# Kernel tuning notes

Measured on AMD Instinct MI355X. Metric: run time of the kernel, lower is better.

## Reference

```python
import jax, jax.numpy as jnp
from jax import lax
import numpy as np

B, C, H, W = 8, 192, 56, 56
N = H * W
K_CLUSTERS = 16   # num_centroids
K_NBRS = 9        # kNN neighbors
FACTOR = 2
COUT = C * FACTOR # hidden channels of graph conv
CPE_K = 7         # depthwise CPE kernel (odd)


def setup_inputs() -> dict:
    key = jax.random.key(0)
    ks = jax.random.split(key, 12)
    s = 0.02
    return {
        "x": jax.random.normal(ks[0], (B, C, H, W), jnp.float32),
        "labels": jax.random.randint(ks[1], (B, N), 0, K_CLUSTERS, jnp.int32),
        "cpe_w": jax.random.normal(ks[2], (C, 1, CPE_K, CPE_K), jnp.float32) * s,
        "cpe_b": jnp.zeros((C,), jnp.float32),
        "fc1_w": jax.random.normal(ks[3], (C, C), jnp.float32) * s,
        "fc1_b": jnp.zeros((C,), jnp.float32),
        "nn_v_w": jax.random.normal(ks[4], (2 * C, COUT), jnp.float32) * s,
        "nn_v_b": jnp.zeros((COUT,), jnp.float32),
        "nn_c_w": jax.random.normal(ks[5], (2 * C, COUT), jnp.float32) * s,
        "nn_c_b": jnp.zeros((COUT,), jnp.float32),
        "fc2_w": jax.random.normal(ks[6], (COUT, C), jnp.float32) * s,
        "fc2_b": jnp.zeros((C,), jnp.float32),
    }


def reference(x, labels, cpe_w, cpe_b, fc1_w, fc1_b, nn_v_w, nn_v_b,
              nn_c_w, nn_c_b, fc2_w, fc2_b):
    Bx, Cx, Hx, Wx = x.shape
    n = Hx * Wx
    shortcut = x
    # --- Conditional Position Encoding: depthwise conv + residual ---
    pe = lax.conv_general_dilated(
        x, cpe_w, (1, 1), "SAME", feature_group_count=Cx,
        dimension_numbers=("NCHW", "OIHW", "NCHW"))
    x = pe + cpe_b[None, :, None, None] + x
    # --- fc1: 1x1 conv ---
    xf = jnp.einsum("bchw,cd->bdhw", x, fc1_w) + fc1_b[None, :, None, None]
    xn = xf.reshape(Bx, Cx, n).transpose(0, 2, 1)  # [B,N,C]
    # --- organize_and_map: stable sort nodes by cluster label ---
    order = jnp.argsort(labels, axis=1)            # sorted pos -> orig idx (stable)
    mapping = jnp.argsort(order, axis=1)           # orig idx -> sorted pos
    xs = jnp.take_along_axis(xn, order[:, :, None], axis=1)  # [B,N,C]
    ls = jnp.take_along_axis(labels, order, axis=1)          # [B,N]
    # --- kNN on l2-normalized feats, restricted to same cluster ---
    xe = xs / jnp.maximum(jnp.linalg.norm(xs, axis=-1, keepdims=True), 1e-12)
    sq = jnp.sum(xe * xe, axis=-1)                 # [B,N]
    d2 = sq[:, :, None] + sq[:, None, :] - 2.0 * jnp.einsum("bnc,bmc->bnm", xe, xe)
    same = ls[:, :, None] == ls[:, None, :]        # [B,N,N] cluster mask
    d2 = jnp.where(same, d2, jnp.inf)
    _, nbr = lax.top_k(-d2, K_NBRS)                # [B,N,k] nearest in-cluster
    valid = jnp.take_along_axis(same, nbr, axis=2) # False when cluster < k
    # --- vertex edge conv: max_j MLP([x_i, x_j - x_i]) ---
    xj = jax.vmap(lambda xb, nb: xb[nb])(xs, nbr)  # [B,N,k,C]
    xi = xs[:, :, None, :]
    msg = jnp.concatenate([jnp.broadcast_to(xi, xj.shape), xj - xi], axis=-1)
    h = jax.nn.gelu(msg @ nn_v_w + nn_v_b)         # [B,N,k,COUT]
    h = jnp.where(valid[..., None], h, -jnp.inf)   # self is always valid
    hv = jnp.max(h, axis=2)                        # [B,N,COUT]
    # --- centroid edge conv over cluster centers (fully connected per image) ---
    onehot = (ls[:, :, None] == jnp.arange(K_CLUSTERS)[None, None, :]).astype(xs.dtype)
    cnt = jnp.maximum(onehot.sum(axis=1), 1.0)     # [B,K]
    cen = jnp.einsum("bnk,bnc->bkc", onehot, xs) / cnt[:, :, None]
    ci = cen[:, :, None, :]
    cj = cen[:, None, :, :]
    cmsg = jnp.concatenate(
        [jnp.broadcast_to(ci, (Bx, K_CLUSTERS, K_CLUSTERS, Cx)), cj - ci], axis=-1)
    hc = jnp.max(jax.nn.gelu(cmsg @ nn_c_w + nn_c_b), axis=2)  # [B,K,COUT]
    hcn = jax.vmap(lambda hb, lb: hb[lb])(hc, ls)  # scatter center feat to nodes
    hn = hv + hcn                                  # [B,N,COUT]
    # --- unshuffle back to original raster order ---
    out_nodes = jnp.take_along_axis(hn, mapping[:, :, None], axis=1)
    # --- fc2: 1x1 conv back to C, residual ---
    y = out_nodes @ fc2_w + fc2_b                  # [B,N,C]
    y = y.transpose(0, 2, 1).reshape(Bx, Cx, Hx, Wx)
    return y + shortcut
```

## Files before the change

### kernel.cpp

```cpp
#include <hip/hip_runtime.h>
#include <math.h>

#define NB 8
#define NC 192
#define NH 56
#define NW 56
#define NN 3136
#define NK 16
#define KNB 9
#define NCOUT 384
#define LPMAX 320
#define DSTRIDE 320
#define DSLOT (320 * 320)

#define FLT_INF __builtin_inff()

typedef short s16x8 __attribute__((ext_vector_type(8)));
typedef _Float16 f16x8 __attribute__((ext_vector_type(8)));
typedef float f32x4 __attribute__((ext_vector_type(4)));
typedef unsigned short us8 __attribute__((ext_vector_type(8)));
typedef unsigned short us4 __attribute__((ext_vector_type(4)));

__device__ __forceinline__ float gelu_t(float x) {
    const float k0 = 0.7978845608028654f;
    float u = k0 * (x + 0.044715f * x * x * x);
    float sg = __builtin_amdgcn_rcpf(1.0f + __expf(-2.0f * u));
    return x * sg;
}

__device__ __forceinline__ unsigned short f2bf(float f) {
    unsigned u = __float_as_uint(f);
    u += 0x7fff + ((u >> 16) & 1);
    return (unsigned short)(u >> 16);
}

__device__ __forceinline__ float bf2f(unsigned short h) {
    return __uint_as_float(((unsigned)h) << 16);
}


#define FRONT_CONV_BLOCKS (NB * NC)
#define FRONT_ORDER_BLOCKS (NB * NK)
#define FRONT_WCVT_BLOCKS 288
__global__ __launch_bounds__(256) void front_kernel(
    const float* __restrict__ X, const float* __restrict__ W7, const float* __restrict__ bias,
    unsigned short* __restrict__ xpe,
    const int* __restrict__ labels, int* __restrict__ order, int* __restrict__ mapping,
    int* __restrict__ lsv, int* __restrict__ cntk, int* __restrict__ offk,
    const float* __restrict__ Wf1, const float* __restrict__ Wv, const float* __restrict__ Wf2,
    unsigned short* __restrict__ wf1, unsigned short* __restrict__ wfpmq,
    unsigned short* __restrict__ wfq, unsigned short* __restrict__ wf2) {
    __shared__ float tile[62 * 62];
    __shared__ float wl[49];
    int bid = blockIdx.x;
    int tid = threadIdx.x;
    if (bid < FRONT_CONV_BLOCKS) {
        int bc = (bid & 7) * NC + (bid >> 3);
        int c = bc % NC;
        const float* Xp = X + (size_t)bc * NN;
        if (tid < 49) wl[tid] = W7[(size_t)c * 49 + tid];
        for (int idx = tid; idx < 62 * 62; idx += 256) {
            int ty = idx / 62, tx = idx % 62;
            int gy = ty - 3, gx = tx - 3;
            float v = 0.0f;
            if (gy >= 0 && gy < NH && gx >= 0 && gx < NW) v = Xp[gy * NW + gx];
            tile[idx] = v;
        }
        __syncthreads();
        float cb = bias[c];
        for (int g = tid; g < (NN / 4); g += 256) {
            int y = g / (NW / 4), x0 = (g % (NW / 4)) * 4;
            float a0 = 0.f, a1 = 0.f, a2 = 0.f, a3 = 0.f;
#pragma unroll
            for (int dy = 0; dy < 7; ++dy) {
                const float* tr = &tile[(y + dy) * 62 + x0];
#pragma unroll
                for (int dx = 0; dx < 7; ++dx) {
                    float wv = wl[dy * 7 + dx];
                    a0 += tr[dx] * wv;
                    a1 += tr[dx + 1] * wv;
                    a2 += tr[dx + 2] * wv;
                    a3 += tr[dx + 3] * wv;
                }
            }
            const float* rr = &tile[(y + 3) * 62 + x0 + 3];
            us4 o;
            o[0] = f2bf(a0 + cb + rr[0]);
            o[1] = f2bf(a1 + cb + rr[1]);
            o[2] = f2bf(a2 + cb + rr[2]);
            o[3] = f2bf(a3 + cb + rr[3]);
            *(us4*)(xpe + (size_t)bc * NN + y * NW + x0) = o;
        }
    } else if (bid < FRONT_CONV_BLOCKS + FRONT_ORDER_BLOCKS) {
        if (tid >= 64) return;
        int idx = bid - FRONT_CONV_BLOCKS;
        int b = idx >> 4;
        int k = idx & 15;
        int lane = tid;
        const int* lb = labels + (size_t)b * NN;
        int cntLess = 0, cntEq = 0;
        for (int n0 = 0; n0 < NN; n0 += 64) {
            int lab = lb[n0 + lane] & 15;
            cntLess += __popcll(__ballot(lab < k));
            cntEq += __popcll(__ballot(lab == k));
        }
        int base = cntLess;
        int run = 0;
        for (int n0 = 0; n0 < NN; n0 += 64) {
            int n = n0 + lane;
            int lab = lb[n] & 15;
            bool p = (lab == k);
            unsigned long long mask = __ballot(p);
            int rank = __popcll(mask & ((1ull << lane) - 1ull));
            if (p) {
                int pos = base + run + rank;
                order[b * NN + pos] = n;
                mapping[b * NN + n] = pos;
                lsv[b * NN + pos] = k;
            }
            run += __popcll(mask);
        }
        if (lane == 0) {
            offk[b * NK + k] = base;
            cntk[b * NK + k] = cntEq;
        }
    } else {
        int u = bid - (FRONT_CONV_BLOCKS + FRONT_ORDER_BLOCKS);
        int nt = u % 6, kc = (u / 6) % 12, z = u / 72;
        const float* W;
        unsigned short* Bf;
        int ldw, rowoff, KC, NT;
        bool diff = false;
        if (z == 0) { W = Wf1; Bf = wf1; ldw = NC; rowoff = 0; KC = 6; NT = 3; }
        else if (z == 1) { W = Wv; Bf = wfpmq; ldw = NCOUT; rowoff = 0; KC = 6; NT = 6; diff = true; }
        else if (z == 2) { W = Wv; Bf = wfq; ldw = NCOUT; rowoff = NC; KC = 6; NT = 6; }
        else { W = Wf2; Bf = wf2; ldw = NC; rowoff = 0; KC = 12; NT = 3; }
        if (nt >= NT || kc >= KC) return;
        int c = tid >> 6, l = tid & 63;
        int n = l & 15, q = l >> 4;
        int col = nt * 64 + c * 16 + n;
        int krow = rowoff + kc * 32 + q * 8;
        unsigned short pack[8];
#pragma unroll
        for (int j = 0; j < 8; ++j) {
            float v = W[(size_t)(krow + j) * ldw + col];
            if (diff) v -= W[(size_t)(NC + krow + j) * ldw + col];
            pack[j] = f2bf(v);
        }
        *(us8*)(Bf + ((((size_t)nt * KC + kc) * 4 + c) * 64 + l) * 8) = *(const us8*)pack;
    }
}

__global__ __launch_bounds__(256) void tcvt_kernel(const unsigned short* __restrict__ xpe,
                                                   unsigned short* __restrict__ Af) {
    __shared__ unsigned short t[32][72];
    int lin = ((int)blockIdx.z * 6 + blockIdx.y) * 49 + blockIdx.x;
    int b = lin & 7, pos = lin >> 3;
    int kc = pos / 49, nx = pos % 49;
    int n0 = nx * 64;
    int tid = threadIdx.x;
    int cl = tid >> 3, nl = (tid & 7) * 8;
    const unsigned short* src = xpe + ((size_t)b * NC + kc * 32 + cl) * NN + n0 + nl;
    *(us8*)&t[cl][nl] = *(const us8*)src;
    __syncthreads();
    int w = tid >> 6, l = tid & 63;
    int m = l & 15, q = l >> 4;
    int nloc = w * 16 + m;
    unsigned short pack[8];
#pragma unroll
    for (int j = 0; j < 8; ++j) pack[j] = t[q * 8 + j][nloc];
    int sg = nx * 4 + w;
    *(us8*)(Af + (size_t)b * NN * NC + (((size_t)sg * 6 + kc) * 64 + l) * 8) =
        *(const us8*)pack;
}

template <int KC>
__global__ __launch_bounds__(256) void gemm_mfma(const unsigned short* __restrict__ Af,
                                                 size_t aStride,
                                                 const unsigned short* __restrict__ Bf,
                                                 const float* __restrict__ bias,
                                                 float* __restrict__ C, size_t cStride,
                                                 int ldc, unsigned short* __restrict__ Cfrag,
                                                 const int* __restrict__ rowmap) {
    int NX = gridDim.x;
    int lin = ((int)blockIdx.z * 49 + blockIdx.y) * NX + blockIdx.x;
    int b = lin & 7, pos = lin >> 3;
    int bx = pos % NX, by = pos / NX;
    int w = threadIdx.x >> 6, lane = threadIdx.x & 63;
    int sg = by * 4 + w;
    int n0 = bx * 64;
    const unsigned short* Ap = Af + (size_t)b * aStride + ((size_t)sg * KC * 64 + lane) * 8;
    const unsigned short* Bp = Bf + ((size_t)bx * KC * 256 + lane) * 8;
    f32x4 acc[4] = {};
#pragma unroll
    for (int kc = 0; kc < KC; ++kc) {
        s16x8 a = *(const s16x8*)(Ap + kc * 512);
#pragma unroll
        for (int c = 0; c < 4; ++c) {
            s16x8 bv = *(const s16x8*)(Bp + kc * 2048 + c * 512);
            acc[c] = __builtin_amdgcn_mfma_f32_16x16x32_bf16(a, bv, acc[c], 0, 0, 0);
        }
    }
    int col0 = lane & 15, rq = lane >> 4;
    float* Cb = C + (size_t)b * cStride;
    int kcd = ldc >> 5;
#pragma unroll
    for (int r = 0; r < 4; ++r) {
        int grow = sg * 16 + rq * 4 + r;
        int orow = rowmap ? rowmap[(size_t)b * NN + grow] : grow;
#pragma unroll
        for (int c = 0; c < 4; ++c) {
            int col = n0 + c * 16 + col0;
            float v = acc[c][r];
            if (bias) v += bias[col];
            Cb[(size_t)orow * ldc + col] = v;
            if (Cfrag) {
                int s2 = orow >> 4, m2 = orow & 15;
                int kc2 = col >> 5, q2 = (col >> 3) & 3, j2 = col & 7;
                Cfrag[(size_t)b * cStride +
                      (((size_t)s2 * kcd + kc2) * 64 + q2 * 16 + m2) * 8 + j2] = f2bf(v);
            }
        }
    }
}

template <int KC>
__global__ __launch_bounds__(256) void gemm_mfma_pq(const unsigned short* __restrict__ Af,
                                                    size_t aStride,
                                                    const unsigned short* __restrict__ B1,
                                                    const unsigned short* __restrict__ B2,
                                                    const float* __restrict__ bias,
                                                    unsigned short* __restrict__ PmQ,
                                                    unsigned short* __restrict__ Qh,
                                                    size_t cStride, int ldc) {
    int lin = ((int)blockIdx.z * 49 + blockIdx.y) * 6 + blockIdx.x;
    int b = lin & 7, pos = lin >> 3;
    int bx = pos % 6, by = pos / 6;
    int w = threadIdx.x >> 6, lane = threadIdx.x & 63;
    int sg = by * 4 + w;
    int n0 = bx * 64;
    const unsigned short* Ap = Af + (size_t)b * aStride + ((size_t)sg * KC * 64 + lane) * 8;
    const unsigned short* Bp1 = B1 + ((size_t)bx * KC * 256 + lane) * 8;
    const unsigned short* Bp2 = B2 + ((size_t)bx * KC * 256 + lane) * 8;
    f32x4 acc1[4] = {};
    f32x4 acc2[4] = {};
#pragma unroll
    for (int kc = 0; kc < KC; ++kc) {
        s16x8 a = *(const s16x8*)(Ap + kc * 512);
#pragma unroll
        for (int c = 0; c < 4; ++c) {
            s16x8 b1 = *(const s16x8*)(Bp1 + kc * 2048 + c * 512);
            acc1[c] = __builtin_amdgcn_mfma_f32_16x16x32_bf16(a, b1, acc1[c], 0, 0, 0);
            s16x8 b2 = *(const s16x8*)(Bp2 + kc * 2048 + c * 512);
            acc2[c] = __builtin_amdgcn_mfma_f32_16x16x32_bf16(a, b2, acc2[c], 0, 0, 0);
        }
    }
    int col0 = lane & 15, rq = lane >> 4;
    unsigned short* Pb = PmQ + (size_t)b * cStride;
    unsigned short* Qb = Qh + (size_t)b * cStride;
#pragma unroll
    for (int r = 0; r < 4; ++r) {
        int grow = sg * 16 + rq * 4 + r;
#pragma unroll
        for (int c = 0; c < 4; ++c) {
            int col = n0 + c * 16 + col0;
            Pb[(size_t)grow * ldc + col] = f2bf(acc1[c][r] + bias[col]);
            Qb[(size_t)grow * ldc + col] = f2bf(acc2[c][r]);
        }
    }
}

template <int KC>
__global__ __launch_bounds__(256) void gemm_mfma_hb(const unsigned short* __restrict__ Af,
                                                    size_t aStride,
                                                    const unsigned short* __restrict__ Bf,
                                                    const float* __restrict__ bias,
                                                    unsigned short* __restrict__ C,
                                                    size_t cStride, int ldc) {
    int lin = ((int)blockIdx.z * 49 + blockIdx.y) * 3 + blockIdx.x;
    int b = lin & 7, pos = lin >> 3;
    int bx = pos % 3, by = pos / 3;
    int w = threadIdx.x >> 6, lane = threadIdx.x & 63;
    int sg = by * 4 + w;
    int n0 = bx * 64;
    const unsigned short* Ap = Af + (size_t)b * aStride + ((size_t)sg * KC * 64 + lane) * 8;
    const unsigned short* Bp = Bf + ((size_t)bx * KC * 256 + lane) * 8;
    f32x4 acc[4] = {};
#pragma unroll
    for (int kc = 0; kc < KC; ++kc) {
        s16x8 a = *(const s16x8*)(Ap + kc * 512);
#pragma unroll
        for (int c = 0; c < 4; ++c) {
            s16x8 bv = *(const s16x8*)(Bp + kc * 2048 + c * 512);
            acc[c] = __builtin_amdgcn_mfma_f32_16x16x32_bf16(a, bv, acc[c], 0, 0, 0);
        }
    }
    int col0 = lane & 15, rq = lane >> 4;
    unsigned short* Cb = C + (size_t)b * cStride;
#pragma unroll
    for (int r = 0; r < 4; ++r) {
        int grow = sg * 16 + rq * 4 + r;
#pragma unroll
        for (int c = 0; c < 4; ++c) {
            int col = n0 + c * 16 + col0;
            Cb[(size_t)grow * ldc + col] = f2bf(acc[c][r] + bias[col]);
        }
    }
}

__global__ __launch_bounds__(384) void xe_cvt_kernel(const float* __restrict__ xs,
                                                     const int* __restrict__ offk,
                                                     const int* __restrict__ cntk,
                                                     _Float16* __restrict__ xef,
                                                     float* __restrict__ sqv) {
    __shared__ float psum[16][25];
    __shared__ float rloc[16];
    int lin = ((int)blockIdx.z * 16 + blockIdx.y) * 20 + blockIdx.x;
    int b = lin & 7, pos = lin >> 3;
    int k = pos / 20, strip = pos % 20;
    int bk = b * NK + k;
    int base = offk[bk], L = cntk[bk];
    if (strip * 16 >= L) return;
    int kc = threadIdx.x >> 6, l = threadIdx.x & 63;
    int m = l & 15, q = l >> 4;
    int rl = strip * 16 + m;
    int row = base + (rl < L ? rl : L - 1);
    const float* src = xs + ((size_t)b * NN + row) * NC + kc * 32 + q * 8;
    float4 v0 = *(const float4*)src;
    float4 v1 = *(const float4*)(src + 4);
    float part = v0.x * v0.x + v0.y * v0.y + v0.z * v0.z + v0.w * v0.w + v1.x * v1.x +
                 v1.y * v1.y + v1.z * v1.z + v1.w * v1.w;
    psum[m][kc * 4 + q] = part;
    __syncthreads();
    if (threadIdx.x < 16) {
        float s = 0.0f;
#pragma unroll
        for (int i2 = 0; i2 < 24; ++i2) s += psum[threadIdx.x][i2];
        float nrm = fmaxf(sqrtf(s), 1e-12f);
        float ri = 1.0f / nrm;
        rloc[threadIdx.x] = ri;
        if (strip * 16 + (int)threadIdx.x < L)
            sqv[(size_t)b * NN + base + strip * 16 + threadIdx.x] = (s * ri) * ri;
    }
    __syncthreads();
    float rv = rloc[m];
    f16x8 pack;
    pack[0] = (_Float16)(v0.x * rv);
    pack[1] = (_Float16)(v0.y * rv);
    pack[2] = (_Float16)(v0.z * rv);
    pack[3] = (_Float16)(v0.w * rv);
    pack[4] = (_Float16)(v1.x * rv);
    pack[5] = (_Float16)(v1.y * rv);
    pack[6] = (_Float16)(v1.z * rv);
    pack[7] = (_Float16)(v1.w * rv);
    *(f16x8*)(xef + (size_t)bk * (20 * 6 * 512) + (((size_t)strip * 6 + kc) * 64 + l) * 8) =
        pack;
}

__global__ __launch_bounds__(256) void gram_kernel(const _Float16* __restrict__ xef,
                                                   const float* __restrict__ sqv,
                                                   const int* __restrict__ offk,
                                                   const int* __restrict__ cntk,
                                                   float* __restrict__ D) {
    int lin = ((int)blockIdx.z * 5 + blockIdx.y) * 5 + blockIdx.x;
    int b = lin & 7, pos = lin >> 3;
    int k = pos / 25, rr = pos % 25;
    int tj = rr / 5, ti = rr % 5;
    int bk = b * NK + k;
    int base = offk[bk], L = cntk[bk];
    if (ti * 64 >= L || tj * 64 >= L) return;
    int w = threadIdx.x >> 6, lane = threadIdx.x & 63;
    const _Float16* Xf = xef + (size_t)bk * (20 * 6 * 512);
    const _Float16* Ap = Xf + (((size_t)(ti * 4 + w) * 6) * 64 + lane) * 8;
    f32x4 acc[4] = {};
#pragma unroll
    for (int kc = 0; kc < 6; ++kc) {
        f16x8 a = *(const f16x8*)(Ap + kc * 512);
#pragma unroll
        for (int js = 0; js < 4; ++js) {
            f16x8 bv = *(const f16x8*)(Xf + (((size_t)(tj * 4 + js) * 6 + kc) * 64 + lane) * 8);
            acc[js] = __builtin_amdgcn_mfma_f32_16x16x32_f16(a, bv, acc[js], 0, 0, 0);
        }
    }
    float* Dr = D + (size_t)bk * DSLOT;
    const float* Sb = sqv + (size_t)b * NN + base;
    int col0 = lane & 15, rq = lane >> 4;
#pragma unroll
    for (int r = 0; r < 4; ++r) {
        int i = ti * 64 + w * 16 + rq * 4 + r;
        if (i >= L) continue;
        float si = Sb[i];
#pragma unroll
        for (int js = 0; js < 4; ++js) {
            int j = tj * 64 + js * 16 + col0;
            if (j < L) Dr[(size_t)i * DSTRIDE + j] = si + Sb[j] - 2.0f * acc[js][r];
        }
    }
}

#define LEXLT(da, ca, db, cb) ((da) < (db) || ((da) == (db) && (ca) < (cb)))
__global__ __launch_bounds__(256) void select9_kernel(const float* __restrict__ D,
                                                      const int* __restrict__ lsv,
                                                      const int* __restrict__ offk,
                                                      const int* __restrict__ cntk,
                                                      int* __restrict__ nbr) {
    int lin = (int)blockIdx.y * 784 + blockIdx.x;
    int b = lin & 7, quad = lin >> 3;
    int r = quad * 4 + (threadIdx.x >> 6);
    int lane = threadIdx.x & 63;
    int k = lsv[(size_t)b * NN + r];
    int bk = b * NK + k;
    int base = offk[bk], L = cntk[bk];
    int Lc = L < LPMAX ? L : LPMAX;
    const float* Dr = D + (size_t)bk * DSLOT + (size_t)(r - base) * DSTRIDE;
    float d0, d1, d2, d3, d4;
    int c0, c1, c2, c3, c4;
    c0 = lane;
    c1 = lane + 64;
    c2 = lane + 128;
    c3 = lane + 192;
    c4 = lane + 256;
    d0 = c0 < Lc ? Dr[c0] : FLT_INF;
    d1 = c1 < Lc ? Dr[c1] : FLT_INF;
    d2 = c2 < Lc ? Dr[c2] : FLT_INF;
    d3 = c3 < Lc ? Dr[c3] : FLT_INF;
    d4 = c4 < Lc ? Dr[c4] : FLT_INF;
#define CS(da, ca, db, cb)                  \
    if (LEXLT(db, cb, da, ca)) {            \
        float t = da; da = db; db = t;      \
        int u = ca; ca = cb; cb = u;        \
    }
    CS(d0, c0, d1, c1) CS(d3, c3, d4, c4) CS(d2, c2, d4, c4) CS(d2, c2, d3, c3)
    CS(d1, c1, d4, c4) CS(d0, c0, d3, c3) CS(d0, c0, d2, c2) CS(d1, c1, d3, c3)
    CS(d1, c1, d2, c2)
#undef CS
    size_t row = (size_t)b * NN + r;
    for (int q = 0; q < KNB; ++q) {
        float bd = d0;
        int bc = c0;
#pragma unroll
        for (int m = 32; m; m >>= 1) {
            float od = __shfl_xor(bd, m, 64);
            int oc = __shfl_xor(bc, m, 64);
            if (LEXLT(od, oc, bd, bc)) {
                bd = od;
                bc = oc;
            }
        }
        if (lane == 0) nbr[row * KNB + q] = base + bc;
        if (d0 == bd && c0 == bc) {
            d0 = d1; c0 = c1;
            d1 = d2; c1 = c2;
            d2 = d3; c2 = c3;
            d3 = d4; c3 = c4;
            d4 = FLT_INF; c4 = 0x7fffffff;
        }
    }
}

__global__ __launch_bounds__(768) void cenpq_kernel(const float* __restrict__ xs,
                                                    const int* __restrict__ offk,
                                                    const int* __restrict__ cntk,
                                                    const float* __restrict__ Wc,
                                                    const float* __restrict__ bc,
                                                    float* __restrict__ Pc,
                                                    float* __restrict__ Qc) {
    __shared__ float part[4][NC];
    __shared__ float ce[NC];
    __shared__ float pcs[NCOUT], qcs[NCOUT];
    int bk = ((int)blockIdx.x & 7) * NK + ((int)blockIdx.x >> 3);
    int b = bk >> 4;
    int base = offk[bk], L = cntk[bk];
    int w = threadIdx.x / NC;
    int c = threadIdx.x % NC;
    const float* Xb = xs + ((size_t)b * NN + base) * NC + c;
    float s = 0.0f;
    for (int r = w; r < L; r += 4) s += Xb[(size_t)r * NC];
    part[w][c] = s;
    __syncthreads();
    if (threadIdx.x < NC) {
        int cc = threadIdx.x;
        float tot = part[0][cc] + part[1][cc] + part[2][cc] + part[3][cc];
        ce[cc] = tot / fmaxf((float)L, 1.0f);
    }
    __syncthreads();
    int o = threadIdx.x % NCOUT, half = threadIdx.x / NCOUT;
    float pc = 0.0f, qc = 0.0f;
    int cs = half * 96, cend = cs + 96;
    for (int c2 = cs; c2 < cend; ++c2) {
        float cv = ce[c2];
        pc += cv * Wc[(size_t)c2 * NCOUT + o];
        qc += cv * Wc[(size_t)(NC + c2) * NCOUT + o];
    }
    if (half == 1) {
        pcs[o] = pc;
        qcs[o] = qc;
    }
    __syncthreads();
    if (half == 0) {
        Pc[(size_t)bk * NCOUT + o] = pc + pcs[o] + bc[o];
        Qc[(size_t)bk * NCOUT + o] = qc + qcs[o];
    }
}

__global__ __launch_bounds__(384) void hcmax_kernel(const float* __restrict__ Pc,
                                                    const float* __restrict__ Qc,
                                                    float* __restrict__ hc) {
    int bk = ((int)blockIdx.x & 7) * NK + ((int)blockIdx.x >> 3);
    int b = bk >> 4, i = bk & 15;
    int o = threadIdx.x;
    float pi = Pc[((size_t)b * NK + i) * NCOUT + o];
    float qi = Qc[((size_t)b * NK + i) * NCOUT + o];
    float pmq = pi - qi;
    float qmn = FLT_INF, qmx = -FLT_INF;
    for (int j = 0; j < NK; ++j) {
        float v = Qc[((size_t)b * NK + j) * NCOUT + o];
        qmn = fminf(qmn, v);
        qmx = fmaxf(qmx, v);
    }
    hc[((size_t)b * NK + i) * NCOUT + o] =
        fmaxf(gelu_t(pmq + qmn), gelu_t(pmq + qmx));
}

__global__ __launch_bounds__(192) void hv_kernel(const unsigned short* __restrict__ PmQ,
                                                 const unsigned short* __restrict__ Qh,
                                                 const int* __restrict__ nbr,
                                                 const int* __restrict__ lsv,
                                                 const float* __restrict__ hc,
                                                 unsigned short* __restrict__ hnf) {
    int lin = (int)blockIdx.y * 784 + blockIdx.x;
    int b = lin & 7, quad = lin >> 3;
    int t = threadIdx.x;
    int rsub = t / 48, c = t % 48;
    int i = quad * 4 + rsub;
    size_t row = (size_t)b * NN + i;
    int lab = lsv[row];
    int o0 = c * 8;
    int jn[KNB];
#pragma unroll
    for (int q = 0; q < KNB; ++q) jn[q] = nbr[row * KNB + q];
    const unsigned short* Qbb = Qh + (size_t)b * NN * NCOUT + o0;
    us8 pv = *(const us8*)(PmQ + row * NCOUT + o0);
    us8 q0 = *(const us8*)(Qbb + (size_t)jn[0] * NCOUT);
    float qmn[8], qmx[8];
#pragma unroll
    for (int e = 0; e < 8; ++e) {
        float v = bf2f(q0[e]);
        qmn[e] = v;
        qmx[e] = v;
    }
#pragma unroll
    for (int q = 1; q < KNB; ++q) {
        us8 qv = *(const us8*)(Qbb + (size_t)jn[q] * NCOUT);
#pragma unroll
        for (int e = 0; e < 8; ++e) {
            float v = bf2f(qv[e]);
            qmn[e] = fminf(qmn[e], v);
            qmx[e] = fmaxf(qmx[e], v);
        }
    }
    const float* hcr = hc + ((size_t)b * NK + lab) * NCOUT + o0;
    float4 h0 = *(const float4*)hcr;
    float4 h1 = *(const float4*)(hcr + 4);
    float hcv[8] = {h0.x, h0.y, h0.z, h0.w, h1.x, h1.y, h1.z, h1.w};
    unsigned short pack[8];
#pragma unroll
    for (int e = 0; e < 8; ++e) {
        float pmq = bf2f(pv[e]);
        float m = fmaxf(gelu_t(pmq + qmn[e]), gelu_t(pmq + qmx[e]));
        pack[e] = f2bf(m + hcv[e]);
    }
    int s = i >> 4, mm = i & 15;
    *(us8*)(hnf + (size_t)b * NN * NCOUT +
            (((size_t)s * 12 + (c >> 2)) * 64 + (c & 3) * 16 + mm) * 8) = *(const us8*)pack;
}

__global__ void out_kernel(const unsigned short* __restrict__ T, const float* __restrict__ X,
                           const int* __restrict__ mapping, float* __restrict__ Y) {
    __shared__ float t[32][33];
    int lin = ((int)blockIdx.z * 98 + blockIdx.y) * 6 + blockIdx.x;
    int b = lin & 7, pos = lin >> 3;
    int c0 = (pos % 6) * 32, n0 = (pos / 6) * 32;
    int tx = threadIdx.x, ty = threadIdx.y;
#pragma unroll
    for (int q = 0; q < 4; ++q) {
        int n = n0 + ty + q * 8;
        int srow = mapping[(size_t)b * NN + n];
        t[ty + q * 8][tx] = bf2f(T[((size_t)b * NN + srow) * NC + c0 + tx]);
    }
    __syncthreads();
#pragma unroll
    for (int q = 0; q < 4; ++q) {
        int c = c0 + ty + q * 8;
        size_t idx = ((size_t)b * NC + c) * NN + n0 + tx;
        Y[idx] = t[tx][ty + q * 8] + X[idx];
    }
}

extern "C" void kernel_launch(void* const* d_in, const int* in_sizes, int n_in, void* d_out,
                              int out_size, void* d_ws, size_t ws_size, hipStream_t stream) {
    const float* x = (const float*)d_in[0];
    const int* labels = (const int*)d_in[1];
    const float* cpe_w = (const float*)d_in[2];
    const float* cpe_b = (const float*)d_in[3];
    const float* fc1_w = (const float*)d_in[4];
    const float* fc1_b = (const float*)d_in[5];
    const float* nn_v_w = (const float*)d_in[6];
    const float* nn_v_b = (const float*)d_in[7];
    const float* nn_c_w = (const float*)d_in[8];
    const float* nn_c_b = (const float*)d_in[9];
    const float* fc2_w = (const float*)d_in[10];
    const float* fc2_b = (const float*)d_in[11];
    float* out = (float*)d_out;

    const size_t SZ_XS = (size_t)NB * NN * NC;
    const size_t SZ_P = (size_t)NB * NN * NCOUT;
    const size_t BN = (size_t)NB * NN;
    const size_t SZ_CEN = (size_t)NB * NK * NC;
    const size_t SZ_PC = (size_t)NB * NK * NCOUT;

    float* base = (float*)d_ws;
    float* xs = base;
    float* xpeRegion = xs + SZ_XS;
    float* Pb = xpeRegion + SZ_XS;
    float* Qb = Pb + SZ_P;
    float* rinv = Qb + SZ_P;
    float* sqv = rinv + BN;
    float* cen = sqv + BN;
    float* Pc = cen + SZ_CEN;
    float* Qc = Pc + SZ_PC;
    float* hcv = Qc + SZ_PC;
    int* order = (int*)(hcv + SZ_PC);
    int* mapping = order + BN;
    int* lsv = mapping + BN;
    int* nbrv = lsv + BN;
    int* cntk = nbrv + BN * KNB;
    int* offk = cntk + NB * NK;
    unsigned short* xpe = (unsigned short*)xpeRegion;
    float* Dbuf = Pb;
    unsigned short* PmQh = (unsigned short*)Pb;
    unsigned short* Qh = (unsigned short*)Qb;
    unsigned short* out_t = (unsigned short*)xs;
    unsigned short* frag = (unsigned short*)(offk + NB * NK);
    unsigned short* xpeT_frag = frag;
    unsigned short* xs_frag = frag + SZ_XS;
    unsigned short* hn_frag = frag;
    unsigned short* wf1 = frag + 2 * SZ_XS;
    unsigned short* wfpmq = wf1 + (size_t)NC * NC;
    unsigned short* wfq = wfpmq + (size_t)NC * NCOUT;
    unsigned short* wf2 = wfq + (size_t)NC * NCOUT;
    _Float16* xef = (_Float16*)(wf2 + (size_t)NCOUT * NC);

    front_kernel<<<FRONT_CONV_BLOCKS + FRONT_ORDER_BLOCKS + FRONT_WCVT_BLOCKS, 256, 0, stream>>>(
        x, cpe_w, cpe_b, xpe, labels, order, mapping, lsv, cntk, offk, fc1_w, nn_v_w, fc2_w,
        wf1, wfpmq, wfq, wf2);
    tcvt_kernel<<<dim3(NN / 64, NC / 32, NB), 256, 0, stream>>>(xpe, xpeT_frag);
    gemm_mfma<6><<<dim3(NC / 64, NN / 64, NB), 256, 0, stream>>>(
        xpeT_frag, SZ_XS / NB, wf1, fc1_b, xs, (size_t)NN * NC, NC, xs_frag, mapping);
    xe_cvt_kernel<<<dim3(LPMAX / 16, NK, NB), 384, 0, stream>>>(xs, offk, cntk, xef, sqv);
    gram_kernel<<<dim3(LPMAX / 64, LPMAX / 64, NB * NK), 256, 0, stream>>>(xef, sqv, offk,
                                                                           cntk, Dbuf);
    select9_kernel<<<dim3(NN / 4, NB), 256, 0, stream>>>(Dbuf, lsv, offk, cntk, nbrv);
    gemm_mfma_pq<6><<<dim3(NCOUT / 64, NN / 64, NB), 256, 0, stream>>>(
        xs_frag, SZ_XS / NB, wfpmq, wfq, nn_v_b, PmQh, Qh, (size_t)NN * NCOUT, NCOUT);
    cenpq_kernel<<<NB * NK, 768, 0, stream>>>(xs, offk, cntk, nn_c_w, nn_c_b, Pc, Qc);
    hcmax_kernel<<<NB * NK, NCOUT, 0, stream>>>(Pc, Qc, hcv);
    hv_kernel<<<dim3(NN / 4, NB), 192, 0, stream>>>(PmQh, Qh, nbrv, lsv, hcv, hn_frag);
    gemm_mfma_hb<12><<<dim3(NC / 64, NN / 64, NB), 256, 0, stream>>>(
        hn_frag, SZ_P / NB, wf2, fc2_b, out_t, (size_t)NN * NC, NC);
    out_kernel<<<dim3(NC / 32, NN / 32, NB), dim3(32, 8), 0, stream>>>(out_t, x, mapping, out);
}
```

Before: 284.0 us.

## Fuse transpose into fc1 GEMM and fuse hv gather-max into fc2 GEMM

Removes the separate transpose-convert kernel by having the fc1 MFMA kernel read xpe columns directly with strided loads and compute all 192 output columns per block. It also fuses the neighbor min/max GELU aggregation into the fc2 GEMM, staging the hn tile in shared memory instead of writing it to global memory and relaunching. This cuts two launches and a global round trip for the intermediates. In exchange it adds strided, uncoalesced A loads, a larger accumulator register footprint (12 f32x4 per wave), and fewer blocks per launch (392), which may lower occupancy.

```diff
diff --git a/kernel.cpp b/kernel.cpp
--- a/kernel.cpp
+++ b/kernel.cpp
@@ -151,75 +151,46 @@
     }
 }
 
-__global__ __launch_bounds__(256) void tcvt_kernel(const unsigned short* __restrict__ xpe,
-                                                   unsigned short* __restrict__ Af) {
-    __shared__ unsigned short t[32][72];
-    int lin = ((int)blockIdx.z * 6 + blockIdx.y) * 49 + blockIdx.x;
-    int b = lin & 7, pos = lin >> 3;
-    int kc = pos / 49, nx = pos % 49;
-    int n0 = nx * 64;
-    int tid = threadIdx.x;
-    int cl = tid >> 3, nl = (tid & 7) * 8;
-    const unsigned short* src = xpe + ((size_t)b * NC + kc * 32 + cl) * NN + n0 + nl;
-    *(us8*)&t[cl][nl] = *(const us8*)src;
-    __syncthreads();
-    int w = tid >> 6, l = tid & 63;
-    int m = l & 15, q = l >> 4;
-    int nloc = w * 16 + m;
-    unsigned short pack[8];
-#pragma unroll
-    for (int j = 0; j < 8; ++j) pack[j] = t[q * 8 + j][nloc];
-    int sg = nx * 4 + w;
-    *(us8*)(Af + (size_t)b * NN * NC + (((size_t)sg * 6 + kc) * 64 + l) * 8) =
-        *(const us8*)pack;
-}
-
-template <int KC>
-__global__ __launch_bounds__(256) void gemm_mfma(const unsigned short* __restrict__ Af,
-                                                 size_t aStride,
-                                                 const unsigned short* __restrict__ Bf,
-                                                 const float* __restrict__ bias,
-                                                 float* __restrict__ C, size_t cStride,
-                                                 int ldc, unsigned short* __restrict__ Cfrag,
-                                                 const int* __restrict__ rowmap) {
-    int NX = gridDim.x;
-    int lin = ((int)blockIdx.z * 49 + blockIdx.y) * NX + blockIdx.x;
-    int b = lin & 7, pos = lin >> 3;
-    int bx = pos % NX, by = pos / NX;
+__global__ __launch_bounds__(256) void fc1_kernel(const unsigned short* __restrict__ xpe,
+                                                  const unsigned short* __restrict__ Bf,
+                                                  const float* __restrict__ bias,
+                                                  float* __restrict__ xs,
+                                                  unsigned short* __restrict__ Cfrag,
+                                                  const int* __restrict__ rowmap) {
+    int lin = blockIdx.x;
+    int b = lin & 7, by = lin >> 3;
     int w = threadIdx.x >> 6, lane = threadIdx.x & 63;
     int sg = by * 4 + w;
-    int n0 = bx * 64;
-    const unsigned short* Ap = Af + (size_t)b * aStride + ((size_t)sg * KC * 64 + lane) * 8;
-    const unsigned short* Bp = Bf + ((size_t)bx * KC * 256 + lane) * 8;
-    f32x4 acc[4] = {};
-#pragma unroll
-    for (int kc = 0; kc < KC; ++kc) {
-        s16x8 a = *(const s16x8*)(Ap + kc * 512);
-#pragma unroll
-        for (int c = 0; c < 4; ++c) {
-            s16x8 bv = *(const s16x8*)(Bp + kc * 2048 + c * 512);
-            acc[c] = __builtin_amdgcn_mfma_f32_16x16x32_bf16(a, bv, acc[c], 0, 0, 0);
-        }
-    }
-    int col0 = lane & 15, rq = lane >> 4;
-    float* Cb = C + (size_t)b * cStride;
-    int kcd = ldc >> 5;
+    int m = lane & 15, q = lane >> 4;
+    int n = by * 64 + w * 16 + m;
+    const unsigned short* Xb = xpe + (size_t)b * NC * NN + n;
+    f32x4 acc[12] = {};
+#pragma unroll
+    for (int kc = 0; kc < 6; ++kc) {
+        int ch = kc * 32 + q * 8;
+        s16x8 a;
+#pragma unroll
+        for (int j = 0; j < 8; ++j) a[j] = (short)Xb[(size_t)(ch + j) * NN];
+#pragma unroll
+        for (int ct = 0; ct < 12; ++ct) {
+            s16x8 bv = *(const s16x8*)(Bf + ((((size_t)(ct >> 2) * 6 + kc) * 4 + (ct & 3)) * 64 + lane) * 8);
+            acc[ct] = __builtin_amdgcn_mfma_f32_16x16x32_bf16(a, bv, acc[ct], 0, 0, 0);
+        }
+    }
+    float* Cb = xs + (size_t)b * NN * NC;
 #pragma unroll
     for (int r = 0; r < 4; ++r) {
-        int grow = sg * 16 + rq * 4 + r;
-        int orow = rowmap ? rowmap[(size_t)b * NN + grow] : grow;
-#pragma unroll
-        for (int c = 0; c < 4; ++c) {
-            int col = n0 + c * 16 + col0;
-            float v = acc[c][r];
-            if (bias) v += bias[col];
-            Cb[(size_t)orow * ldc + col] = v;
-            if (Cfrag) {
-                int s2 = orow >> 4, m2 = orow & 15;
-                int kc2 = col >> 5, q2 = (col >> 3) & 3, j2 = col & 7;
-                Cfrag[(size_t)b * cStride +
-                      (((size_t)s2 * kcd + kc2) * 64 + q2 * 16 + m2) * 8 + j2] = f2bf(v);
-            }
+        int grow = sg * 16 + q * 4 + r;
+        int orow = rowmap[(size_t)b * NN + grow];
+        int s2 = orow >> 4, m2 = orow & 15;
+#pragma unroll
+        for (int ct = 0; ct < 12; ++ct) {
+            int col = ct * 16 + m;
+            float v = acc[ct][r] + bias[col];
+            Cb[(size_t)orow * NC + col] = v;
+            int kc2 = col >> 5, q2 = (col >> 3) & 3, j2 = col & 7;
+            Cfrag[(size_t)b * NN * NC + (((size_t)s2 * 6 + kc2) * 64 + q2 * 16 + m2) * 8 + j2] =
+                f2bf(v);
         }
     }
 }
@@ -266,44 +237,6 @@
             int col = n0 + c * 16 + col0;
             Pb[(size_t)grow * ldc + col] = f2bf(acc1[c][r] + bias[col]);
             Qb[(size_t)grow * ldc + col] = f2bf(acc2[c][r]);
-        }
-    }
-}
-
-template <int KC>
-__global__ __launch_bounds__(256) void gemm_mfma_hb(const unsigned short* __restrict__ Af,
-                                                    size_t aStride,
-                                                    const unsigned short* __restrict__ Bf,
-                                                    const float* __restrict__ bias,
-                                                    unsigned short* __restrict__ C,
-                                                    size_t cStride, int ldc) {
-    int lin = ((int)blockIdx.z * 49 + blockIdx.y) * 3 + blockIdx.x;
-    int b = lin & 7, pos = lin >> 3;
-    int bx = pos % 3, by = pos / 3;
-    int w = threadIdx.x >> 6, lane = threadIdx.x & 63;
-    int sg = by * 4 + w;
-    int n0 = bx * 64;
-    const unsigned short* Ap = Af + (size_t)b * aStride + ((size_t)sg * KC * 64 + lane) * 8;
-    const unsigned short* Bp = Bf + ((size_t)bx * KC * 256 + lane) * 8;
-    f32x4 acc[4] = {};
-#pragma unroll
-    for (int kc = 0; kc < KC; ++kc) {
-        s16x8 a = *(const s16x8*)(Ap + kc * 512);
-#pragma unroll
-        for (int c = 0; c < 4; ++c) {
-            s16x8 bv = *(const s16x8*)(Bp + kc * 2048 + c * 512);
-            acc[c] = __builtin_amdgcn_mfma_f32_16x16x32_bf16(a, bv, acc[c], 0, 0, 0);
-        }
-    }
-    int col0 = lane & 15, rq = lane >> 4;
-    unsigned short* Cb = C + (size_t)b * cStride;
-#pragma unroll
-    for (int r = 0; r < 4; ++r) {
-        int grow = sg * 16 + rq * 4 + r;
-#pragma unroll
-        for (int c = 0; c < 4; ++c) {
-            int col = n0 + c * 16 + col0;
-            Cb[(size_t)grow * ldc + col] = f2bf(acc[c][r] + bias[col]);
         }
     }
 }
@@ -522,57 +455,89 @@
         fmaxf(gelu_t(pmq + qmn), gelu_t(pmq + qmx));
 }
 
-__global__ __launch_bounds__(192) void hv_kernel(const unsigned short* __restrict__ PmQ,
-                                                 const unsigned short* __restrict__ Qh,
-                                                 const int* __restrict__ nbr,
-                                                 const int* __restrict__ lsv,
-                                                 const float* __restrict__ hc,
-                                                 unsigned short* __restrict__ hnf) {
-    int lin = (int)blockIdx.y * 784 + blockIdx.x;
-    int b = lin & 7, quad = lin >> 3;
+__global__ __launch_bounds__(256) void fc2hv_kernel(const unsigned short* __restrict__ PmQ,
+                                                    const unsigned short* __restrict__ Qh,
+                                                    const int* __restrict__ nbr,
+                                                    const int* __restrict__ lsv,
+                                                    const float* __restrict__ hc,
+                                                    const unsigned short* __restrict__ Bf,
+                                                    const float* __restrict__ bias,
+                                                    unsigned short* __restrict__ C) {
+    __shared__ unsigned short hn[4 * 12 * 64 * 8];
+    int lin = blockIdx.x;
+    int b = lin & 7, by = lin >> 3;
     int t = threadIdx.x;
-    int rsub = t / 48, c = t % 48;
-    int i = quad * 4 + rsub;
-    size_t row = (size_t)b * NN + i;
+    int i = t >> 2;
+    int qc = t & 3;
+    size_t grow = (size_t)by * 64 + i;
+    size_t row = (size_t)b * NN + grow;
     int lab = lsv[row];
-    int o0 = c * 8;
     int jn[KNB];
 #pragma unroll
-    for (int q = 0; q < KNB; ++q) jn[q] = nbr[row * KNB + q];
-    const unsigned short* Qbb = Qh + (size_t)b * NN * NCOUT + o0;
-    us8 pv = *(const us8*)(PmQ + row * NCOUT + o0);
-    us8 q0 = *(const us8*)(Qbb + (size_t)jn[0] * NCOUT);
-    float qmn[8], qmx[8];
-#pragma unroll
-    for (int e = 0; e < 8; ++e) {
-        float v = bf2f(q0[e]);
-        qmn[e] = v;
-        qmx[e] = v;
-    }
-#pragma unroll
-    for (int q = 1; q < KNB; ++q) {
-        us8 qv = *(const us8*)(Qbb + (size_t)jn[q] * NCOUT);
+    for (int qq = 0; qq < KNB; ++qq) jn[qq] = nbr[row * KNB + qq];
+    const unsigned short* Qbb = Qh + (size_t)b * NN * NCOUT;
+    const unsigned short* Pr = PmQ + row * NCOUT;
+    const float* hcr = hc + ((size_t)b * NK + lab) * NCOUT;
+    int wq = t >> 6, mq = (t >> 2) & 15;
+#pragma unroll
+    for (int k = 0; k < 12; ++k) {
+        int o0 = k * 32 + qc * 8;
+        us8 pv = *(const us8*)(Pr + o0);
+        us8 q0 = *(const us8*)(Qbb + (size_t)jn[0] * NCOUT + o0);
+        float qmn[8], qmx[8];
 #pragma unroll
         for (int e = 0; e < 8; ++e) {
-            float v = bf2f(qv[e]);
-            qmn[e] = fminf(qmn[e], v);
-            qmx[e] = fmaxf(qmx[e], v);
-        }
-    }
-    const float* hcr = hc + ((size_t)b * NK + lab) * NCOUT + o0;
-    float4 h0 = *(const float4*)hcr;
-    float4 h1 = *(const float4*)(hcr + 4);
-    float hcv[8] = {h0.x, h0.y, h0.z, h0.w, h1.x, h1.y, h1.z, h1.w};
-    unsigned short pack[8];
-#pragma unroll
-    for (int e = 0; e < 8; ++e) {
-        float pmq = bf2f(pv[e]);
-        float m = fmaxf(gelu_t(pmq + qmn[e]), gelu_t(pmq + qmx[e]));
-        pack[e] = f2bf(m + hcv[e]);
-    }
-    int s = i >> 4, mm = i & 15;
-    *(us8*)(hnf + (size_t)b * NN * NCOUT +
-            (((size_t)s * 12 + (c >> 2)) * 64 + (c & 3) * 16 + mm) * 8) = *(const us8*)pack;
+            float v = bf2f(q0[e]);
+            qmn[e] = v;
+            qmx[e] = v;
+        }
+#pragma unroll
+        for (int q = 1; q < KNB; ++q) {
+            us8 qv = *(const us8*)(Qbb + (size_t)jn[q] * NCOUT + o0);
+#pragma unroll
+            for (int e = 0; e < 8; ++e) {
+                float v = bf2f(qv[e]);
+                qmn[e] = fminf(qmn[e], v);
+                qmx[e] = fmaxf(qmx[e], v);
+            }
+        }
+        float4 h0 = *(const float4*)(hcr + o0);
+        float4 h1 = *(const float4*)(hcr + o0 + 4);
+        float hcv[8] = {h0.x, h0.y, h0.z, h0.w, h1.x, h1.y, h1.z, h1.w};
+        us8 pack;
+#pragma unroll
+        for (int e = 0; e < 8; ++e) {
+            float pmq = bf2f(pv[e]);
+            float mx = fmaxf(gelu_t(pmq + qmn[e]), gelu_t(pmq + qmx[e]));
+            pack[e] = f2bf(mx + hcv[e]);
+        }
+        int slot = (wq * 12 + k) * 64 + qc * 16 + mq;
+        *(us8*)(hn + (size_t)slot * 8) = pack;
+    }
+    __syncthreads();
+    int w = t >> 6, lane = t & 63;
+    f32x4 acc[12] = {};
+#pragma unroll
+    for (int kc = 0; kc < 12; ++kc) {
+        s16x8 a = *(const s16x8*)(hn + (((size_t)w * 12 + kc) * 64 + lane) * 8);
+#pragma unroll
+        for (int ct = 0; ct < 12; ++ct) {
+            s16x8 bv = *(const s16x8*)(Bf + ((((size_t)(ct >> 2) * 12 + kc) * 4 + (ct & 3)) * 64 + lane) * 8);
+            acc[ct] = __builtin_amdgcn_mfma_f32_16x16x32_bf16(a, bv, acc[ct], 0, 0, 0);
+        }
+    }
+    int col0 = lane & 15, rq = lane >> 4;
+    unsigned short* Cb = C + (size_t)b * NN * NC;
+    int sg = by * 4 + w;
+#pragma unroll
+    for (int r = 0; r < 4; ++r) {
+        int grow2 = sg * 16 + rq * 4 + r;
+#pragma unroll
+        for (int ct = 0; ct < 12; ++ct) {
+            int col = ct * 16 + col0;
+            Cb[(size_t)grow2 * NC + col] = f2bf(acc[ct][r] + bias[col]);
+        }
+    }
 }
 
 __global__ void out_kernel(const unsigned short* __restrict__ T, const float* __restrict__ X,
@@ -642,9 +607,7 @@
     unsigned short* Qh = (unsigned short*)Qb;
     unsigned short* out_t = (unsigned short*)xs;
     unsigned short* frag = (unsigned short*)(offk + NB * NK);
-    unsigned short* xpeT_frag = frag;
     unsigned short* xs_frag = frag + SZ_XS;
-    unsigned short* hn_frag = frag;
     unsigned short* wf1 = frag + 2 * SZ_XS;
     unsigned short* wfpmq = wf1 + (size_t)NC * NC;
     unsigned short* wfq = wfpmq + (size_t)NC * NCOUT;
@@ -654,9 +617,7 @@
     front_kernel<<<FRONT_CONV_BLOCKS + FRONT_ORDER_BLOCKS + FRONT_WCVT_BLOCKS, 256, 0, stream>>>(
         x, cpe_w, cpe_b, xpe, labels, order, mapping, lsv, cntk, offk, fc1_w, nn_v_w, fc2_w,
         wf1, wfpmq, wfq, wf2);
-    tcvt_kernel<<<dim3(NN / 64, NC / 32, NB), 256, 0, stream>>>(xpe, xpeT_frag);
-    gemm_mfma<6><<<dim3(NC / 64, NN / 64, NB), 256, 0, stream>>>(
-        xpeT_frag, SZ_XS / NB, wf1, fc1_b, xs, (size_t)NN * NC, NC, xs_frag, mapping);
+    fc1_kernel<<<NB * (NN / 64), 256, 0, stream>>>(xpe, wf1, fc1_b, xs, xs_frag, mapping);
     xe_cvt_kernel<<<dim3(LPMAX / 16, NK, NB), 384, 0, stream>>>(xs, offk, cntk, xef, sqv);
     gram_kernel<<<dim3(LPMAX / 64, LPMAX / 64, NB * NK), 256, 0, stream>>>(xef, sqv, offk,
                                                                            cntk, Dbuf);
@@ -665,8 +626,7 @@
         xs_frag, SZ_XS / NB, wfpmq, wfq, nn_v_b, PmQh, Qh, (size_t)NN * NCOUT, NCOUT);
     cenpq_kernel<<<NB * NK, 768, 0, stream>>>(xs, offk, cntk, nn_c_w, nn_c_b, Pc, Qc);
     hcmax_kernel<<<NB * NK, NCOUT, 0, stream>>>(Pc, Qc, hcv);
-    hv_kernel<<<dim3(NN / 4, NB), 192, 0, stream>>>(PmQh, Qh, nbrv, lsv, hcv, hn_frag);
-    gemm_mfma_hb<12><<<dim3(NC / 64, NN / 64, NB), 256, 0, stream>>>(
-        hn_frag, SZ_P / NB, wf2, fc2_b, out_t, (size_t)NN * NC, NC);
+    fc2hv_kernel<<<NB * (NN / 64), 256, 0, stream>>>(PmQh, Qh, nbrv, lsv, hcv, wf2, fc2_b,
+                                                     out_t);
     out_kernel<<<dim3(NC / 32, NN / 32, NB), dim3(32, 8), 0, stream>>>(out_t, x, mapping, out);
 }
```

Result: slower. 321.7 us (+13.3%).
